# Kernel tuning notes

Hardware: AMD Instinct MI355X
Metric: run time of the kernel (lower is better)

## Reference

```python
import jax, jax.numpy as jnp
import numpy as np


def setup_inputs() -> dict:
    key = jax.random.key(0)
    kq, kk, kv = jax.random.split(key, 3)
    B, N, H, D = 1, 4096, 16, 64
    q = jax.random.normal(kq, (B, N, H, D), dtype=jnp.float32)
    k = jax.random.normal(kk, (B, N, H, D), dtype=jnp.float32)
    v = jax.random.normal(kv, (B, N, H, D), dtype=jnp.float32)
    return {"q": q, "k": k, "v": v}


def reference(q, k, v):
    # q, k, v: [b, n, h, d]
    d = q.shape[-1]
    scale = 1.0 / jnp.sqrt(jnp.asarray(d, dtype=q.dtype))
    # scores: [b, h, n_q, n_k]
    scores = jnp.einsum("bqhd,bkhd->bhqk", q, k) * scale
    attn = jax.nn.softmax(scores, axis=-1)
    # output back in [b, n, h, d] layout
    out = jnp.einsum("bhqk,bkhd->bqhd", attn, v)
    return out
```

## Files before the change

kernel.cpp:

```cpp
#include <hip/hip_runtime.h>
#include <hip/hip_bf16.h>

#define H 16
#define D 64
#define NSEQ 4096
#define BM 128
#define BN 64
#define NT (NSEQ / BN)

typedef __attribute__((ext_vector_type(8))) short bf16x8;
typedef __attribute__((ext_vector_type(4))) short short4v;
typedef __attribute__((ext_vector_type(4))) float f32x4;
typedef __attribute__((ext_vector_type(4))) float f4v;

union BF8 { bf16x8 v; unsigned u[4]; };
union S4  { short4v s; unsigned u[2]; };

static __device__ __forceinline__ unsigned pk2(float lo, float hi) {
    __hip_bfloat162 h = __float22bfloat162_rn(float2{lo, hi});
    unsigned u;
    __builtin_memcpy(&u, &h, 4);
    return u;
}

static __device__ __forceinline__ float fexp2(float x) {
#if __has_builtin(__builtin_amdgcn_exp2f)
    return __builtin_amdgcn_exp2f(x);
#else
    return exp2f(x);
#endif
}

#define TO_GBL(p) ((const __attribute__((address_space(1))) int*)(unsigned long long)(p))
#define TO_LDS(p) ((__attribute__((address_space(3))) int*)(unsigned int)(unsigned long long)(p))

__global__ void prep(const float* __restrict__ k, const float* __restrict__ v,
                     short* __restrict__ kb, short* __restrict__ vt) {
    __shared__ short L[64 * 72];
    const int h = blockIdx.y, n0 = blockIdx.x * 64, t = threadIdx.x;
    const int rw = t >> 4, c4 = (t & 15) * 4;
    #pragma unroll
    for (int it = 0; it < 4; ++it) {
        const int row = rw + it * 16;
        const size_t gro = ((size_t)(n0 + row) * H + h) * D + c4;
        f4v kf = *(const f4v*)(k + gro);
        S4 ks;
        ks.u[0] = pk2(kf[0], kf[1]);
        ks.u[1] = pk2(kf[2], kf[3]);
        *(short4v*)(kb + ((size_t)h * NSEQ + n0 + row) * D + c4) = ks.s;

        f4v vf = *(const f4v*)(v + gro);
        S4 vs;
        vs.u[0] = pk2(vf[0], vf[1]);
        vs.u[1] = pk2(vf[2], vf[3]);
        *(short4v*)&L[row * 72 + c4] = vs.s;
    }
    __syncthreads();
    const int tr = t & 15, tc = t >> 4;
    const int r0 = tr * 4, d0 = tc * 4;
    short4v ra[4];
    #pragma unroll
    for (int i = 0; i < 4; ++i) {
        const int s = r0 + i, s32 = s & 31, base32 = (s >> 5) * 32;
        const int phys = base32 + ((s32 >> 3) * 4 + (s32 & 3) + 16 * ((s32 >> 2) & 1));
        ra[i] = *(const short4v*)&L[phys * 72 + d0];
    }
    #pragma unroll
    for (int jj = 0; jj < 4; ++jj) {
        short4v o4 = (short4v){ra[0][jj], ra[1][jj], ra[2][jj], ra[3][jj]};
        *(short4v*)(vt + ((size_t)(h * D + d0 + jj)) * NSEQ + n0 + r0) = o4;
    }
}

__global__ __launch_bounds__(256, 2)
void attn_fwd(const float* __restrict__ q, const short* __restrict__ kb,
              const short* __restrict__ vtb, float* __restrict__ out)
{
    const int h     = blockIdx.y;
    const int qbase = blockIdx.x * BM;
    const int tid   = threadIdx.x;
    const int wave  = tid >> 6;
    const int lane  = tid & 63;
    const int lm    = lane & 15;
    const int quad  = lane >> 4;
    const int sw    = lm & 7;

    __shared__ short Kt[2][BN * D];
    __shared__ short Vt[2][BN * D];

    const float c1 = 0.18033688011112042f;

    bf16x8 bq[2][2];
    #pragma unroll
    for (int g = 0; g < 2; ++g) {
        const int qrow = qbase + wave * 32 + g * 16 + lm;
        #pragma unroll
        for (int kc = 0; kc < 2; ++kc) {
            const float* qp = q + ((size_t)qrow * H + h) * D + kc * 32 + quad * 8;
            f4v q0 = *(const f4v*)qp;
            f4v q1 = *(const f4v*)(qp + 4);
            BF8 b;
            b.u[0] = pk2(q0[0] * c1, q0[1] * c1); b.u[1] = pk2(q0[2] * c1, q0[3] * c1);
            b.u[2] = pk2(q1[0] * c1, q1[1] * c1); b.u[3] = pk2(q1[2] * c1, q1[3] * c1);
            bq[g][kc] = b.v;
        }
    }

    BF8 ones;
    ones.u[0] = ones.u[1] = ones.u[2] = ones.u[3] = 0x3F803F80u;

    const f32x4 fz = (f32x4){0.f, 0.f, 0.f, 0.f};
    f32x4 o[2][4];
    #pragma unroll
    for (int g = 0; g < 2; ++g)
        #pragma unroll
        for (int mb = 0; mb < 4; ++mb) o[g][mb] = fz;
    f32x4 lacc[2];
    lacc[0] = fz; lacc[1] = fz;

    const int ci0 = (wave * 2 + 0) * 64 + lane;
    const int ci1 = (wave * 2 + 1) * 64 + lane;
    const int kr0 = ci0 >> 3, kp0 = (ci0 & 7) ^ (kr0 & 7);
    const int kr1 = ci1 >> 3, kp1 = (ci1 & 7) ^ (kr1 & 7);

    const short* kh = kb  + (size_t)h * NSEQ * D;
    const short* vh = vtb + (size_t)h * D * NSEQ;
    const short* pkA = kh + (size_t)kr0 * D + kp0 * 8;
    const short* pkB = kh + (size_t)kr1 * D + kp1 * 8;
    const short* pvA = vh + (size_t)kr0 * NSEQ + kp0 * 8;
    const short* pvB = vh + (size_t)kr1 * NSEQ + kp1 * 8;

    auto issue = [&](int b) {
        __builtin_amdgcn_global_load_lds(TO_GBL(pkA), TO_LDS(&Kt[b][(wave * 2 + 0) * 512]), 16, 0, 0);
        __builtin_amdgcn_global_load_lds(TO_GBL(pkB), TO_LDS(&Kt[b][(wave * 2 + 1) * 512]), 16, 0, 0);
        __builtin_amdgcn_global_load_lds(TO_GBL(pvA), TO_LDS(&Vt[b][(wave * 2 + 0) * 512]), 16, 0, 0);
        __builtin_amdgcn_global_load_lds(TO_GBL(pvB), TO_LDS(&Vt[b][(wave * 2 + 1) * 512]), 16, 0, 0);
        pkA += BN * D; pkB += BN * D; pvA += BN; pvB += BN;
    };

    const int posK0 = ((0 + quad) ^ sw) * 8;
    const int posK1 = ((4 + quad) ^ sw) * 8;

    auto compute = [&](int b) {
        const short* K_ = Kt[b];
        const short* V_ = Vt[b];
        f32x4 st[2][4];

        #pragma unroll
        for (int nb = 0; nb < 4; ++nb) {
            bf16x8 kf0 = *(const bf16x8*)&K_[(nb * 16 + lm) * 64 + posK0];
            bf16x8 kf1 = *(const bf16x8*)&K_[(nb * 16 + lm) * 64 + posK1];
            #pragma unroll
            for (int g = 0; g < 2; ++g) {
                st[g][nb] = __builtin_amdgcn_mfma_f32_16x16x32_bf16(kf0, bq[g][0], fz, 0, 0, 0);
                st[g][nb] = __builtin_amdgcn_mfma_f32_16x16x32_bf16(kf1, bq[g][1], st[g][nb], 0, 0, 0);
            }
        }

        #pragma unroll
        for (int g = 0; g < 2; ++g)
            #pragma unroll
            for (int nb = 0; nb < 4; ++nb)
                #pragma unroll
                for (int r = 0; r < 4; ++r)
                    st[g][nb][r] = fexp2(st[g][nb][r]);

        BF8 pb[2][2];
        #pragma unroll
        for (int g = 0; g < 2; ++g)
            #pragma unroll
            for (int c = 0; c < 2; ++c) {
                pb[g][c].u[0] = pk2(st[g][2 * c][0],     st[g][2 * c][1]);
                pb[g][c].u[1] = pk2(st[g][2 * c][2],     st[g][2 * c][3]);
                pb[g][c].u[2] = pk2(st[g][2 * c + 1][0], st[g][2 * c + 1][1]);
                pb[g][c].u[3] = pk2(st[g][2 * c + 1][2], st[g][2 * c + 1][3]);
            }

        #pragma unroll
        for (int g = 0; g < 2; ++g) {
            lacc[g] = __builtin_amdgcn_mfma_f32_16x16x32_bf16(ones.v, pb[g][0].v, lacc[g], 0, 0, 0);
            lacc[g] = __builtin_amdgcn_mfma_f32_16x16x32_bf16(ones.v, pb[g][1].v, lacc[g], 0, 0, 0);
        }

        #pragma unroll
        for (int c = 0; c < 2; ++c) {
            const int pos = ((c * 4 + quad) ^ sw) * 8;
            #pragma unroll
            for (int mb = 0; mb < 4; ++mb) {
                bf16x8 vf = *(const bf16x8*)&V_[(mb * 16 + lm) * 64 + pos];
                #pragma unroll
                for (int g = 0; g < 2; ++g)
                    o[g][mb] = __builtin_amdgcn_mfma_f32_16x16x32_bf16(vf, pb[g][c].v, o[g][mb], 0, 0, 0);
            }
        }
    };

    issue(0);

    for (int it = 0; it < NT; it += 2) {
        __syncthreads();
        if (it + 1 < NT) issue(1);
        compute(0);
        __syncthreads();
        if (it + 2 < NT) issue(0);
        compute(1);
    }

    #pragma unroll
    for (int g = 0; g < 2; ++g) {
        const float inv = 1.0f / lacc[g][0];
        const int qrow = qbase + wave * 32 + g * 16 + lm;
        float* op = out + ((size_t)qrow * H + h) * D + quad * 4;
        #pragma unroll
        for (int mb = 0; mb < 4; ++mb) {
            f4v w;
            #pragma unroll
            for (int r = 0; r < 4; ++r) w[r] = o[g][mb][r] * inv;
            *(f4v*)(op + mb * 16) = w;
        }
    }
}

extern "C" void kernel_launch(void* const* d_in, const int* in_sizes, int n_in,
                              void* d_out, int out_size, void* d_ws, size_t ws_size,
                              hipStream_t stream) {
    const float* q = (const float*)d_in[0];
    const float* k = (const float*)d_in[1];
    const float* v = (const float*)d_in[2];
    float* out = (float*)d_out;

    short* kb = (short*)d_ws;
    short* vt = kb + (size_t)H * NSEQ * D;

    prep<<<dim3(NSEQ / 64, H), dim3(256), 0, stream>>>(k, v, kb, vt);
    attn_fwd<<<dim3(NSEQ / BM, H), dim3(256), 0, stream>>>(q, kb, vt, out);
}
```

Before: 167.7 us.

## Deepen K/V prefetch to four LDS stages, remap blocks per XCD, add MFMA priority

Replaces the two-buffer K/V LDS ring with a four-stage ring. Three tiles stay in flight, using explicit vmcnt waits and raw barriers instead of __syncthreads. The grid is flattened and block indices are remapped so each group of blocks on the same XCD shares heads, aiming for better L2 reuse of K/V. s_setprio raises wave priority around the MFMA sections. LDS use doubles to 64KB per block, which may limit occupancy to two blocks per CU, and the hand-written waitcnt logic depends on load counts being exact.

```diff
diff --git a/kernel.cpp b/kernel.cpp
--- a/kernel.cpp
+++ b/kernel.cpp
@@ -76,8 +76,11 @@
 void attn_fwd(const float* __restrict__ q, const short* __restrict__ kb,
               const short* __restrict__ vtb, float* __restrict__ out)
 {
-    const int h     = blockIdx.y;
-    const int qbase = blockIdx.x * BM;
+    const int lin   = blockIdx.x;
+    const int idx   = lin >> 3;
+    const int h     = (lin & 7) * 2 + (idx >> 5);
+    const int qbase = (idx & 31) * BM;
+
     const int tid   = threadIdx.x;
     const int wave  = tid >> 6;
     const int lane  = tid & 63;
@@ -85,8 +88,8 @@
     const int quad  = lane >> 4;
     const int sw    = lm & 7;
 
-    __shared__ short Kt[2][BN * D];
-    __shared__ short Vt[2][BN * D];
+    __shared__ short Kt[4][BN * D];
+    __shared__ short Vt[4][BN * D];
 
     const float c1 = 0.18033688011112042f;
 
@@ -146,6 +149,7 @@
         const short* V_ = Vt[b];
         f32x4 st[2][4];
 
+        __builtin_amdgcn_s_setprio(1);
         #pragma unroll
         for (int nb = 0; nb < 4; ++nb) {
             bf16x8 kf0 = *(const bf16x8*)&K_[(nb * 16 + lm) * 64 + posK0];
@@ -156,6 +160,7 @@
                 st[g][nb] = __builtin_amdgcn_mfma_f32_16x16x32_bf16(kf1, bq[g][1], st[g][nb], 0, 0, 0);
             }
         }
+        __builtin_amdgcn_s_setprio(0);
 
         #pragma unroll
         for (int g = 0; g < 2; ++g)
@@ -176,6 +181,7 @@
                 pb[g][c].u[3] = pk2(st[g][2 * c + 1][2], st[g][2 * c + 1][3]);
             }
 
+        __builtin_amdgcn_s_setprio(1);
         #pragma unroll
         for (int g = 0; g < 2; ++g) {
             lacc[g] = __builtin_amdgcn_mfma_f32_16x16x32_bf16(ones.v, pb[g][0].v, lacc[g], 0, 0, 0);
@@ -193,18 +199,26 @@
                     o[g][mb] = __builtin_amdgcn_mfma_f32_16x16x32_bf16(vf, pb[g][c].v, o[g][mb], 0, 0, 0);
             }
         }
+        __builtin_amdgcn_s_setprio(0);
     };
 
-    issue(0);
-
-    for (int it = 0; it < NT; it += 2) {
-        __syncthreads();
-        if (it + 1 < NT) issue(1);
-        compute(0);
-        __syncthreads();
-        if (it + 2 < NT) issue(0);
-        compute(1);
-    }
+#define WAITV8 asm volatile("s_waitcnt vmcnt(8)" ::: "memory")
+#define WAITV4 asm volatile("s_waitcnt vmcnt(4)" ::: "memory")
+#define WAITV0 asm volatile("s_waitcnt vmcnt(0)" ::: "memory")
+#define BARRIER() do { __builtin_amdgcn_s_barrier(); asm volatile("" ::: "memory"); } while (0)
+
+    issue(0); issue(1); issue(2);
+
+    for (int it = 0; it < NT - 4; it += 4) {
+        WAITV8; BARRIER(); issue(3); compute(0);
+        WAITV8; BARRIER(); issue(0); compute(1);
+        WAITV8; BARRIER(); issue(1); compute(2);
+        WAITV8; BARRIER(); issue(2); compute(3);
+    }
+    WAITV8; BARRIER(); issue(3); compute(0);
+    WAITV8; BARRIER(); compute(1);
+    WAITV4; BARRIER(); compute(2);
+    WAITV0; BARRIER(); compute(3);
 
     #pragma unroll
     for (int g = 0; g < 2; ++g) {
@@ -233,5 +247,5 @@
     short* vt = kb + (size_t)H * NSEQ * D;
 
     prep<<<dim3(NSEQ / 64, H), dim3(256), 0, stream>>>(k, v, kb, vt);
-    attn_fwd<<<dim3(NSEQ / BM, H), dim3(256), 0, stream>>>(q, kb, vt, out);
-}
+    attn_fwd<<<dim3((NSEQ / BM) * H), dim3(256), 0, stream>>>(q, kb, vt, out);
+}
```

Measured after the change: 167.7 us. Within noise of the previous version (-0.0%).
